# Kernel tuning notes

Hardware: AMD Instinct MI355X
Metric: run time of the kernel (lower is better)

Reference implementation:

```python
import jax, jax.numpy as jnp
import numpy as np

LTA_W = 0.015  # constant EMA weight (buffer in the torch module)


def setup_inputs() -> dict:
    key = jax.random.key(0)
    wave = jax.random.normal(key, (256, 60000, 3), dtype=jnp.float32)
    return {"wave": wave}


def reference(wave):
    # EMA recurrence: lta[t] = lta[t-1] + w * (x[t] - lta[t-1])
    # Implemented as a time-major lax.scan; carry shape [B, C].
    B, T, C = wave.shape
    w = jnp.asarray(LTA_W, dtype=wave.dtype)
    x_tm = jnp.swapaxes(wave, 0, 1)  # [T, B, C]

    def step(carry, x_t):
        carry = carry + w * (x_t - carry)
        return carry, carry

    _, ys = jax.lax.scan(step, jnp.zeros((B, C), dtype=wave.dtype), x_tm)
    return jnp.swapaxes(ys, 0, 1)  # [B, T, C]
```

## Files before the change

kernel.cpp:

```cpp
#include <hip/hip_runtime.h>


#define T_LEN    60000
#define BATCH    256
#define CH       3
#define NBLK_ROW 8
#define SEG      7500
#define WARM     512
#define LPT      12
#define TS       (256 * LPT)
#define NTILES   3
#define TILE_F   (TS * CH)
#define F4PT     (LPT * CH / 4)

__global__ __launch_bounds__(256) void lta_kernel(const float* __restrict__ x,
                                                  float* __restrict__ out) {
    __shared__ float tile[TILE_F];
    __shared__ float waveA[4], waveV0[4], waveV1[4], waveV2[4];
    __shared__ float carry[CH];

    const int tid  = threadIdx.x;
    const int lane = tid & 63;
    const int wv   = tid >> 6;

    const int blk = blockIdx.x;
    const int b   = blk / NBLK_ROW;
    const int q   = blk % NBLK_ROW;

    const int r0 = q * SEG;
    const int r1 = r0 + SEG;
    const int w0 = (r0 >= WARM) ? (r0 - WARM) : 0;

    const float w  = 0.015f;
    const float a  = 1.0f - w;
    const float a4 = (a * a) * (a * a);

    const float* __restrict__ rowx = x   + (size_t)b * (T_LEN * CH);
    float* __restrict__       rowo = out + (size_t)b * (T_LEN * CH);

    if (tid == 0) { carry[0] = 0.f; carry[1] = 0.f; carry[2] = 0.f; }
    __syncthreads();

    for (int tix = 0; tix < NTILES; ++tix) {
        const int s0 = w0 + tix * TS;
        if (s0 >= r1) break;

        const float C0 = carry[0], C1 = carry[1], C2 = carry[2];

        const int valid_end = (s0 + TS < T_LEN) ? (s0 + TS) : T_LEN;
        const int bound_f4  = ((valid_end - s0) * CH) >> 2;
        {
            const float4* __restrict__ gx = (const float4*)(rowx + (size_t)s0 * CH);
            float4* __restrict__ lt = (float4*)tile;
            #pragma unroll
            for (int j = 0; j < TILE_F / 4 / 256; ++j) {
                int f4 = j * 256 + tid;
                if (f4 < bound_f4) lt[f4] = gx[f4];
            }
        }
        __syncthreads();

        const int t_lo = s0 + LPT * tid;
        int Li = r1 - t_lo;
        Li = (Li < 0) ? 0 : (Li > LPT ? LPT : Li);
        const int ng = Li >> 2;

        const float4* __restrict__ lp = (const float4*)tile + tid * F4PT;
        float y0 = 0.f, y1 = 0.f, y2 = 0.f;
        for (int g = 0; g < ng; ++g) {
            float4 A4 = lp[3 * g + 0];
            float4 B4 = lp[3 * g + 1];
            float4 C4 = lp[3 * g + 2];
            y0 = fmaf(w, A4.x - y0, y0); y1 = fmaf(w, A4.y - y1, y1); y2 = fmaf(w, A4.z - y2, y2);
            y0 = fmaf(w, A4.w - y0, y0); y1 = fmaf(w, B4.x - y1, y1); y2 = fmaf(w, B4.y - y2, y2);
            y0 = fmaf(w, B4.z - y0, y0); y1 = fmaf(w, B4.w - y1, y1); y2 = fmaf(w, C4.x - y2, y2);
            y0 = fmaf(w, C4.y - y0, y0); y1 = fmaf(w, C4.z - y1, y1); y2 = fmaf(w, C4.w - y2, y2);
        }
        float AL = 1.0f;
        for (int g = 0; g < ng; ++g) AL *= a4;

        float As = AL, V0 = y0, V1 = y1, V2 = y2;
        #pragma unroll
        for (int d = 1; d < 64; d <<= 1) {
            float Au = __shfl_up(As, d, 64);
            float u0 = __shfl_up(V0, d, 64);
            float u1 = __shfl_up(V1, d, 64);
            float u2 = __shfl_up(V2, d, 64);
            if (lane >= d) {
                V0 = fmaf(As, u0, V0);
                V1 = fmaf(As, u1, V1);
                V2 = fmaf(As, u2, V2);
                As = As * Au;
            }
        }
        if (lane == 63) { waveA[wv] = As; waveV0[wv] = V0; waveV1[wv] = V1; waveV2[wv] = V2; }
        __syncthreads();

        float Ae = __shfl_up(As, 1, 64);
        float e0 = __shfl_up(V0, 1, 64);
        float e1 = __shfl_up(V1, 1, 64);
        float e2 = __shfl_up(V2, 1, 64);
        if (lane == 0) { Ae = 1.f; e0 = 0.f; e1 = 0.f; e2 = 0.f; }

        float Ap = 1.f, p0 = 0.f, p1 = 0.f, p2 = 0.f;
        for (int k = 0; k < wv; ++k) {
            float Ak = waveA[k];
            p0 = fmaf(Ak, p0, waveV0[k]);
            p1 = fmaf(Ak, p1, waveV1[k]);
            p2 = fmaf(Ak, p2, waveV2[k]);
            Ap *= Ak;
        }

        float Y0 = fmaf(Ae, fmaf(Ap, C0, p0), e0);
        float Y1 = fmaf(Ae, fmaf(Ap, C1, p1), e1);
        float Y2 = fmaf(Ae, fmaf(Ap, C2, p2), e2);

        if (tid == 255) {
            carry[0] = fmaf(As, fmaf(Ap, C0, p0), V0);
            carry[1] = fmaf(As, fmaf(Ap, C1, p1), V1);
            carry[2] = fmaf(As, fmaf(Ap, C2, p2), V2);
        }

        float4* __restrict__ lpw = (float4*)tile + tid * F4PT;
        y0 = Y0; y1 = Y1; y2 = Y2;
        for (int g = 0; g < ng; ++g) {
            float4 A4 = lpw[3 * g + 0];
            float4 B4 = lpw[3 * g + 1];
            float4 C4 = lpw[3 * g + 2];
            float4 D, E, F;
            y0 = fmaf(w, A4.x - y0, y0);  D.x = y0;
            y1 = fmaf(w, A4.y - y1, y1);  D.y = y1;
            y2 = fmaf(w, A4.z - y2, y2);  D.z = y2;
            y0 = fmaf(w, A4.w - y0, y0);  D.w = y0;
            y1 = fmaf(w, B4.x - y1, y1);  E.x = y1;
            y2 = fmaf(w, B4.y - y2, y2);  E.y = y2;
            y0 = fmaf(w, B4.z - y0, y0);  E.z = y0;
            y1 = fmaf(w, B4.w - y1, y1);  E.w = y1;
            y2 = fmaf(w, C4.x - y2, y2);  F.x = y2;
            y0 = fmaf(w, C4.y - y0, y0);  F.y = y0;
            y1 = fmaf(w, C4.z - y1, y1);  F.z = y1;
            y2 = fmaf(w, C4.w - y2, y2);  F.w = y2;
            lpw[3 * g + 0] = D;
            lpw[3 * g + 1] = E;
            lpw[3 * g + 2] = F;
        }
        __syncthreads();

        {
            const int slo = (s0 > r0) ? s0 : r0;
            const int shi = (s0 + TS < r1) ? (s0 + TS) : r1;
            const int lo_f4 = ((slo - s0) * CH) >> 2;
            const int hi_f4 = ((shi - s0) * CH) >> 2;
            float4* __restrict__ go = (float4*)(rowo + (size_t)s0 * CH);
            const float4* __restrict__ lt = (const float4*)tile;
            #pragma unroll
            for (int j = 0; j < TILE_F / 4 / 256; ++j) {
                int f4 = j * 256 + tid;
                if (f4 >= lo_f4 && f4 < hi_f4) go[f4] = lt[f4];
            }
        }
        __syncthreads();
    }
}

extern "C" void kernel_launch(void* const* d_in, const int* in_sizes, int n_in,
                              void* d_out, int out_size, void* d_ws, size_t ws_size,
                              hipStream_t stream) {
    const float* x = (const float*)d_in[0];
    float* out = (float*)d_out;

    const int grid = BATCH * NBLK_ROW;
    lta_kernel<<<grid, 256, 0, stream>>>(x, out);
}
```

Measured before the change: 321.4 us.

## Read and write global memory directly per thread, drop LDS tile staging

Removes the shared-memory tile. Each thread now loads its 12 timesteps directly from global memory, and in the second pass re-reads them and writes outputs straight to global. Cross-tile carries are kept in registers in every thread by folding all four wave aggregates, with the wave scratch double-buffered by parity, so two of the barriers per tile go away. Per-thread float4 accesses are strided by 48 bytes, so coalescing gets worse and each input is read from global twice, relying on cache hits. Launch bounds now ask for higher occupancy.

After: 465.5 us. 44.8% more time.

```diff
diff --git a/kernel.cpp b/kernel.cpp
--- a/kernel.cpp
+++ b/kernel.cpp
@@ -10,14 +10,10 @@
 #define LPT      12
 #define TS       (256 * LPT)
 #define NTILES   3
-#define TILE_F   (TS * CH)
-#define F4PT     (LPT * CH / 4)
 
-__global__ __launch_bounds__(256) void lta_kernel(const float* __restrict__ x,
-                                                  float* __restrict__ out) {
-    __shared__ float tile[TILE_F];
-    __shared__ float waveA[4], waveV0[4], waveV1[4], waveV2[4];
-    __shared__ float carry[CH];
+__global__ __launch_bounds__(256, 8) void lta_kernel(const float* __restrict__ x,
+                                                     float* __restrict__ out) {
+    __shared__ float wA[2][4], wV0[2][4], wV1[2][4], wV2[2][4];
 
     const int tid  = threadIdx.x;
     const int lane = tid & 63;
@@ -38,39 +34,25 @@
     const float* __restrict__ rowx = x   + (size_t)b * (T_LEN * CH);
     float* __restrict__       rowo = out + (size_t)b * (T_LEN * CH);
 
-    if (tid == 0) { carry[0] = 0.f; carry[1] = 0.f; carry[2] = 0.f; }
-    __syncthreads();
+    float C0 = 0.f, C1 = 0.f, C2 = 0.f;
 
     for (int tix = 0; tix < NTILES; ++tix) {
         const int s0 = w0 + tix * TS;
         if (s0 >= r1) break;
-
-        const float C0 = carry[0], C1 = carry[1], C2 = carry[2];
-
-        const int valid_end = (s0 + TS < T_LEN) ? (s0 + TS) : T_LEN;
-        const int bound_f4  = ((valid_end - s0) * CH) >> 2;
-        {
-            const float4* __restrict__ gx = (const float4*)(rowx + (size_t)s0 * CH);
-            float4* __restrict__ lt = (float4*)tile;
-            #pragma unroll
-            for (int j = 0; j < TILE_F / 4 / 256; ++j) {
-                int f4 = j * 256 + tid;
-                if (f4 < bound_f4) lt[f4] = gx[f4];
-            }
-        }
-        __syncthreads();
+        const int par = tix & 1;
 
         const int t_lo = s0 + LPT * tid;
         int Li = r1 - t_lo;
         Li = (Li < 0) ? 0 : (Li > LPT ? LPT : Li);
         const int ng = Li >> 2;
 
-        const float4* __restrict__ lp = (const float4*)tile + tid * F4PT;
+        const float4* __restrict__ gp =
+            (const float4*)(rowx + (size_t)t_lo * CH);
         float y0 = 0.f, y1 = 0.f, y2 = 0.f;
         for (int g = 0; g < ng; ++g) {
-            float4 A4 = lp[3 * g + 0];
-            float4 B4 = lp[3 * g + 1];
-            float4 C4 = lp[3 * g + 2];
+            float4 A4 = gp[3 * g + 0];
+            float4 B4 = gp[3 * g + 1];
+            float4 C4 = gp[3 * g + 2];
             y0 = fmaf(w, A4.x - y0, y0); y1 = fmaf(w, A4.y - y1, y1); y2 = fmaf(w, A4.z - y2, y2);
             y0 = fmaf(w, A4.w - y0, y0); y1 = fmaf(w, B4.x - y1, y1); y2 = fmaf(w, B4.y - y2, y2);
             y0 = fmaf(w, B4.z - y0, y0); y1 = fmaf(w, B4.w - y1, y1); y2 = fmaf(w, C4.x - y2, y2);
@@ -93,7 +75,9 @@
                 As = As * Au;
             }
         }
-        if (lane == 63) { waveA[wv] = As; waveV0[wv] = V0; waveV1[wv] = V1; waveV2[wv] = V2; }
+        if (lane == 63) {
+            wA[par][wv] = As; wV0[par][wv] = V0; wV1[par][wv] = V1; wV2[par][wv] = V2;
+        }
         __syncthreads();
 
         float Ae = __shfl_up(As, 1, 64);
@@ -103,63 +87,59 @@
         if (lane == 0) { Ae = 1.f; e0 = 0.f; e1 = 0.f; e2 = 0.f; }
 
         float Ap = 1.f, p0 = 0.f, p1 = 0.f, p2 = 0.f;
-        for (int k = 0; k < wv; ++k) {
-            float Ak = waveA[k];
-            p0 = fmaf(Ak, p0, waveV0[k]);
-            p1 = fmaf(Ak, p1, waveV1[k]);
-            p2 = fmaf(Ak, p2, waveV2[k]);
-            Ap *= Ak;
+        float At = 1.f, q0 = 0.f, q1 = 0.f, q2 = 0.f;
+        #pragma unroll
+        for (int k = 0; k < 4; ++k) {
+            float Ak = wA[par][k];
+            float k0 = wV0[par][k], k1 = wV1[par][k], k2 = wV2[par][k];
+            if (k < wv) {
+                p0 = fmaf(Ak, p0, k0);
+                p1 = fmaf(Ak, p1, k1);
+                p2 = fmaf(Ak, p2, k2);
+                Ap *= Ak;
+            }
+            q0 = fmaf(Ak, q0, k0);
+            q1 = fmaf(Ak, q1, k1);
+            q2 = fmaf(Ak, q2, k2);
+            At *= Ak;
         }
 
-        float Y0 = fmaf(Ae, fmaf(Ap, C0, p0), e0);
-        float Y1 = fmaf(Ae, fmaf(Ap, C1, p1), e1);
-        float Y2 = fmaf(Ae, fmaf(Ap, C2, p2), e2);
+        const float Y0 = fmaf(Ae, fmaf(Ap, C0, p0), e0);
+        const float Y1 = fmaf(Ae, fmaf(Ap, C1, p1), e1);
+        const float Y2 = fmaf(Ae, fmaf(Ap, C2, p2), e2);
 
-        if (tid == 255) {
-            carry[0] = fmaf(As, fmaf(Ap, C0, p0), V0);
-            carry[1] = fmaf(As, fmaf(Ap, C1, p1), V1);
-            carry[2] = fmaf(As, fmaf(Ap, C2, p2), V2);
-        }
+        C0 = fmaf(At, C0, q0);
+        C1 = fmaf(At, C1, q1);
+        C2 = fmaf(At, C2, q2);
 
-        float4* __restrict__ lpw = (float4*)tile + tid * F4PT;
-        y0 = Y0; y1 = Y1; y2 = Y2;
-        for (int g = 0; g < ng; ++g) {
-            float4 A4 = lpw[3 * g + 0];
-            float4 B4 = lpw[3 * g + 1];
-            float4 C4 = lpw[3 * g + 2];
-            float4 D, E, F;
-            y0 = fmaf(w, A4.x - y0, y0);  D.x = y0;
-            y1 = fmaf(w, A4.y - y1, y1);  D.y = y1;
-            y2 = fmaf(w, A4.z - y2, y2);  D.z = y2;
-            y0 = fmaf(w, A4.w - y0, y0);  D.w = y0;
-            y1 = fmaf(w, B4.x - y1, y1);  E.x = y1;
-            y2 = fmaf(w, B4.y - y2, y2);  E.y = y2;
-            y0 = fmaf(w, B4.z - y0, y0);  E.z = y0;
-            y1 = fmaf(w, B4.w - y1, y1);  E.w = y1;
-            y2 = fmaf(w, C4.x - y2, y2);  F.x = y2;
-            y0 = fmaf(w, C4.y - y0, y0);  F.y = y0;
-            y1 = fmaf(w, C4.z - y1, y1);  F.z = y1;
-            y2 = fmaf(w, C4.w - y2, y2);  F.w = y2;
-            lpw[3 * g + 0] = D;
-            lpw[3 * g + 1] = E;
-            lpw[3 * g + 2] = F;
-        }
-        __syncthreads();
-
-        {
-            const int slo = (s0 > r0) ? s0 : r0;
-            const int shi = (s0 + TS < r1) ? (s0 + TS) : r1;
-            const int lo_f4 = ((slo - s0) * CH) >> 2;
-            const int hi_f4 = ((shi - s0) * CH) >> 2;
-            float4* __restrict__ go = (float4*)(rowo + (size_t)s0 * CH);
-            const float4* __restrict__ lt = (const float4*)tile;
-            #pragma unroll
-            for (int j = 0; j < TILE_F / 4 / 256; ++j) {
-                int f4 = j * 256 + tid;
-                if (f4 >= lo_f4 && f4 < hi_f4) go[f4] = lt[f4];
+        if (ng > 0 && (t_lo + 4 * ng) > r0) {
+            float4* __restrict__ go = (float4*)(rowo + (size_t)t_lo * CH);
+            const int fb = 3 * t_lo;
+            const int f0 = 3 * r0;
+            y0 = Y0; y1 = Y1; y2 = Y2;
+            for (int g = 0; g < ng; ++g) {
+                float4 A4 = gp[3 * g + 0];
+                float4 B4 = gp[3 * g + 1];
+                float4 C4 = gp[3 * g + 2];
+                float4 D, E, F;
+                y0 = fmaf(w, A4.x - y0, y0);  D.x = y0;
+                y1 = fmaf(w, A4.y - y1, y1);  D.y = y1;
+                y2 = fmaf(w, A4.z - y2, y2);  D.z = y2;
+                y0 = fmaf(w, A4.w - y0, y0);  D.w = y0;
+                y1 = fmaf(w, B4.x - y1, y1);  E.x = y1;
+                y2 = fmaf(w, B4.y - y2, y2);  E.y = y2;
+                y0 = fmaf(w, B4.z - y0, y0);  E.z = y0;
+                y1 = fmaf(w, B4.w - y1, y1);  E.w = y1;
+                y2 = fmaf(w, C4.x - y2, y2);  F.x = y2;
+                y0 = fmaf(w, C4.y - y0, y0);  F.y = y0;
+                y1 = fmaf(w, C4.z - y1, y1);  F.z = y1;
+                y2 = fmaf(w, C4.w - y2, y2);  F.w = y2;
+                const int fg = fb + 12 * g;
+                if (fg      >= f0) go[3 * g + 0] = D;
+                if (fg + 4  >= f0) go[3 * g + 1] = E;
+                if (fg + 8  >= f0) go[3 * g + 2] = F;
             }
         }
-        __syncthreads();
     }
 }
 
```
